# Kernel optimization log

Measured on AMD Instinct MI355X. Metric: run time of the kernel, lower is better.

## Reference

```python
import jax, jax.numpy as jnp
import numpy as np

H = 512

def _lstm_cell(x, h, c, Wih, Whh, bih, bhh):
    # PyTorch LSTMCell: gates ordered i, f, g, o
    g = x @ Wih.T + bih + h @ Whh.T + bhh
    i, f, gg, o = jnp.split(g, 4, axis=-1)
    i = jax.nn.sigmoid(i)
    f = jax.nn.sigmoid(f)
    gg = jnp.tanh(gg)
    o = jax.nn.sigmoid(o)
    c_new = f * c + i * gg
    h_new = o * jnp.tanh(c_new)
    return h_new, c_new


def setup_inputs() -> dict:
    key = jax.random.key(0)
    ks = jax.random.split(key, 12)
    B, T = 16, 6574
    s1 = 1.0 / np.sqrt(H)
    u = lambda k, shape: jax.random.uniform(k, shape, jnp.float32, -s1, s1)
    return {
        "input": jax.random.normal(ks[0], (B, T, 2), jnp.float32),
        "W_ih1": u(ks[1], (4 * H, 2)),
        "W_hh1": u(ks[2], (4 * H, H)),
        "b_ih1": u(ks[3], (4 * H,)),
        "b_hh1": u(ks[4], (4 * H,)),
        "W_ih2": u(ks[5], (4 * H, H)),
        "W_hh2": u(ks[6], (4 * H, H)),
        "b_ih2": u(ks[7], (4 * H,)),
        "b_hh2": u(ks[8], (4 * H,)),
        "W_out": u(ks[9], (1, H)),
        "b_out": u(ks[10], (1,)),
    }


def reference(input, W_ih1, W_hh1, b_ih1, b_hh1, W_ih2, W_hh2, b_ih2, b_hh2, W_out, b_out):
    B = input.shape[0]
    h1 = jnp.zeros((B, H), input.dtype)
    c1 = jnp.zeros((B, H), input.dtype)
    h2 = jnp.zeros((B, H), input.dtype)
    c2 = jnp.zeros((B, H), input.dtype)

    def step(carry, x_t):
        h1, c1, h2, c2 = carry
        h1, c1 = _lstm_cell(x_t, h1, c1, W_ih1, W_hh1, b_ih1, b_hh1)
        h2, c2 = _lstm_cell(h1, h2, c2, W_ih2, W_hh2, b_ih2, b_hh2)
        out_t = h2 @ W_out.T + b_out  # [B, 1]
        return (h1, c1, h2, c2), out_t

    xs = jnp.swapaxes(input, 0, 1)  # [T, B, 2]
    _, outs = jax.lax.scan(step, (h1, c1, h2, c2), xs)
    return jnp.swapaxes(outs, 0, 1)  # [B, T, 1]
```

## Files before the change

kernel.cpp:

```cpp
#include <hip/hip_runtime.h>
#include <math.h>

#define NWG  256
#define NTHR 256
#define AGT __HIP_MEMORY_SCOPE_AGENT

#define O_W2  0
#define O_W1  16384
#define O_U   24576
#define O_WX  33280
#define O_B1  33312
#define O_B2  33328
#define O_WO  33344
#define O_XS  33348
#define O_G1  33364
#define O_G2  33492
#define O_C1  33620
#define O_C2  33652
#define LDS_FLOATS 33684

union U64F2 { unsigned long long u; float f[2]; };

__global__ void ws_init_kernel(unsigned* flags, float* h1g, float* h2g,
                               float* out, const float* bout, int n_out) {
    int i = blockIdx.x * blockDim.x + threadIdx.x;
    int n = gridDim.x * blockDim.x;
    float bo = bout[0];
    for (int j = i; j < NWG; j += n) flags[j] = 0u;
    for (int j = i; j < 16384; j += n) { h1g[j] = 0.0f; h2g[j] = 0.0f; }
    for (int j = i; j < n_out; j += n) out[j] = bo;
}

__device__ __forceinline__ float sigm(float x) { return 1.0f / (1.0f + __expf(-x)); }
__device__ __forceinline__ float tanh_fast(float x) { return 2.0f / (1.0f + __expf(-2.0f * x)) - 1.0f; }

__device__ __forceinline__ void gbar(unsigned* flags, int wg, int tid, unsigned ph) {
    __syncthreads();
    asm volatile("s_waitcnt vmcnt(0)" ::: "memory");
    const int half = wg & 1;
    if (tid == 0)
        __hip_atomic_store(&flags[(half << 7) + (wg >> 1)], ph, __ATOMIC_RELAXED, AGT);
    if (tid < 32) {
        const unsigned long long* f64 = (const unsigned long long*)flags + (half << 6);
        bool done;
        do {
            unsigned long long v0 = __hip_atomic_load(&f64[2 * tid],     __ATOMIC_RELAXED, AGT);
            unsigned long long v1 = __hip_atomic_load(&f64[2 * tid + 1], __ATOMIC_RELAXED, AGT);
            done = ((unsigned)v0 >= ph) && ((unsigned)(v0 >> 32) >= ph) &&
                   ((unsigned)v1 >= ph) && ((unsigned)(v1 >> 32) >= ph);
            if (!__all(done)) __builtin_amdgcn_s_sleep(1);
        } while (!__all(done));
    }
    __syncthreads();
}

__global__ __launch_bounds__(NTHR, 1) void lstm_kernel(
    const float* __restrict__ xin,  const float* __restrict__ Wih1,
    const float* __restrict__ Whh1, const float* __restrict__ bih1,
    const float* __restrict__ bhh1, const float* __restrict__ Wih2,
    const float* __restrict__ Whh2, const float* __restrict__ bih2,
    const float* __restrict__ bhh2, const float* __restrict__ Wout,
    const float* __restrict__ bout, float* __restrict__ out,
    unsigned* __restrict__ flags, float* __restrict__ h1g,
    float* __restrict__ h2g, float* __restrict__ outred, int T)
{
    __shared__ float lds[LDS_FLOATS];
    const int tid = threadIdx.x;
    const int wg  = blockIdx.x;
    const int bh  = wg & 1;
    const int jg  = wg >> 1;
    const int j0  = jg * 4;
    const int bd  = bh * 8 + (jg & 7);
    const int jh  = jg >> 3;

    for (int idx = tid; idx < 2048; idx += NTHR) {
        int r = idx >> 7, c4 = idx & 127;
        int grow = (r >> 2) * 512 + j0 + (r & 3);
        *(float4*)&lds[O_W1 + r * 512 + c4 * 4] = *(const float4*)&Whh1[grow * 512 + c4 * 4];
    }
    for (int idx = tid; idx < 4096; idx += NTHR) {
        int r = idx >> 8, c4 = idx & 255;
        int grow = (r >> 2) * 512 + j0 + (r & 3);
        int k = c4 * 4;
        const float* src = (k < 512) ? &Wih2[grow * 512 + k] : &Whh2[grow * 512 + (k - 512)];
        *(float4*)&lds[O_W2 + r * 1024 + k] = *(const float4*)src;
    }
    if (tid < 32) {
        int r = tid >> 1, grow = (r >> 2) * 512 + j0 + (r & 3);
        lds[O_WX + tid] = Wih1[grow * 2 + (tid & 1)];
    }
    if (tid < 16) {
        int grow = (tid >> 2) * 512 + j0 + (tid & 3);
        lds[O_B1 + tid] = bih1[grow] + bhh1[grow];
        lds[O_B2 + tid] = bih2[grow] + bhh2[grow];
    }
    if (tid < 4) lds[O_WO + tid] = Wout[j0 + tid];
    if (tid < 32) { lds[O_C1 + tid] = 0.0f; lds[O_C2 + tid] = 0.0f; }
    __syncthreads();

    const int wv = tid >> 6;
    const int ks = tid & 63;
    unsigned ph = 0;

    float xreg = 0.0f;
    if (tid < 16 && T > 0) {
        int b = tid >> 1, cm = tid & 1;
        xreg = xin[((bh * 8 + b) * (long)T + 0) * 2 + cm];
    }

    for (int s = 0; s <= T; ++s) {
        const int p = s & 1, pq = p ^ 1;

        if (s >= 2 && tid == 0) {
            const unsigned long long* row64 =
                (const unsigned long long*)(outred + pq * 2048 + bd * 128 + jh * 8);
            U64F2 v0; v0.u = __hip_atomic_load(&row64[0], __ATOMIC_RELAXED, AGT);
            U64F2 v1; v1.u = __hip_atomic_load(&row64[1], __ATOMIC_RELAXED, AGT);
            U64F2 v2; v2.u = __hip_atomic_load(&row64[2], __ATOMIC_RELAXED, AGT);
            U64F2 v3; v3.u = __hip_atomic_load(&row64[3], __ATOMIC_RELAXED, AGT);
            float sum = (v0.f[0] + v0.f[1]) + (v1.f[0] + v1.f[1])
                      + (v2.f[0] + v2.f[1]) + (v3.f[0] + v3.f[1]);
            atomicAdd(&out[bd * T + (s - 2)], sum);
        }

        if (tid < 16) {
            if (s < T) lds[O_XS + tid] = xreg;
            if (s + 1 < T) {
                int b = tid >> 1, cm = tid & 1;
                xreg = xin[((bh * 8 + b) * (long)T + (s + 1)) * 2 + cm];
            }
        }

        {
            const float* srcb = (tid < 128)
                ? (h1g + pq * 8192 + (bh * 8) * 512 + tid * 4)
                : (h2g + pq * 8192 + (bh * 8) * 512 + (tid - 128) * 4);
            float4 r0, r1, r2, r3, r4, r5, r6, r7;
            asm volatile(
                "global_load_dwordx4 %0, %8, off sc0 sc1\n\t"
                "global_load_dwordx4 %1, %9, off sc0 sc1\n\t"
                "global_load_dwordx4 %2, %10, off sc0 sc1\n\t"
                "global_load_dwordx4 %3, %11, off sc0 sc1\n\t"
                "global_load_dwordx4 %4, %12, off sc0 sc1\n\t"
                "global_load_dwordx4 %5, %13, off sc0 sc1\n\t"
                "global_load_dwordx4 %6, %14, off sc0 sc1\n\t"
                "global_load_dwordx4 %7, %15, off sc0 sc1\n\t"
                "s_waitcnt vmcnt(0)"
                : "=&v"(r0), "=&v"(r1), "=&v"(r2), "=&v"(r3),
                  "=&v"(r4), "=&v"(r5), "=&v"(r6), "=&v"(r7)
                : "v"(srcb),        "v"(srcb + 512),  "v"(srcb + 1024), "v"(srcb + 1536),
                  "v"(srcb + 2048), "v"(srcb + 2560), "v"(srcb + 3072), "v"(srcb + 3584)
                : "memory");
            const int d = tid * 4;
            *(float4*)&lds[O_U + 0 * 1024 + d] = r0;
            *(float4*)&lds[O_U + 1 * 1024 + d] = r1;
            *(float4*)&lds[O_U + 2 * 1024 + d] = r2;
            *(float4*)&lds[O_U + 3 * 1024 + d] = r3;
            *(float4*)&lds[O_U + 4 * 1024 + d] = r4;
            *(float4*)&lds[O_U + 5 * 1024 + d] = r5;
            *(float4*)&lds[O_U + 6 * 1024 + d] = r6;
            *(float4*)&lds[O_U + 7 * 1024 + d] = r7;
        }
        __syncthreads();

        float a1[4][8], a2[4][8];
        #pragma unroll
        for (int r = 0; r < 4; ++r)
            #pragma unroll
            for (int b = 0; b < 8; ++b) { a1[r][b] = 0.0f; a2[r][b] = 0.0f; }
        {
            const float* W2b = &lds[O_W2 + wv * 4096];
            const float* W1b = &lds[O_W1 + wv * 2048];
            #pragma unroll
            for (int c = 0; c < 4; ++c) {
                const int k = ks * 4 + c * 256;
                float4 u0 = *(const float4*)&W2b[k];
                float4 u1 = *(const float4*)&W2b[1024 + k];
                float4 u2 = *(const float4*)&W2b[2048 + k];
                float4 u3 = *(const float4*)&W2b[3072 + k];
                float4 w0, w1, w2, w3;
                if (c < 2) {
                    w0 = *(const float4*)&W1b[k];
                    w1 = *(const float4*)&W1b[512 + k];
                    w2 = *(const float4*)&W1b[1024 + k];
                    w3 = *(const float4*)&W1b[1536 + k];
                }
                #pragma unroll
                for (int b = 0; b < 8; ++b) {
                    float4 h = *(const float4*)&lds[O_U + b * 1024 + k];
                    a2[0][b] = fmaf(u0.x,h.x,fmaf(u0.y,h.y,fmaf(u0.z,h.z,fmaf(u0.w,h.w,a2[0][b]))));
                    a2[1][b] = fmaf(u1.x,h.x,fmaf(u1.y,h.y,fmaf(u1.z,h.z,fmaf(u1.w,h.w,a2[1][b]))));
                    a2[2][b] = fmaf(u2.x,h.x,fmaf(u2.y,h.y,fmaf(u2.z,h.z,fmaf(u2.w,h.w,a2[2][b]))));
                    a2[3][b] = fmaf(u3.x,h.x,fmaf(u3.y,h.y,fmaf(u3.z,h.z,fmaf(u3.w,h.w,a2[3][b]))));
                    if (c < 2) {
                        a1[0][b] = fmaf(w0.x,h.x,fmaf(w0.y,h.y,fmaf(w0.z,h.z,fmaf(w0.w,h.w,a1[0][b]))));
                        a1[1][b] = fmaf(w1.x,h.x,fmaf(w1.y,h.y,fmaf(w1.z,h.z,fmaf(w1.w,h.w,a1[1][b]))));
                        a1[2][b] = fmaf(w2.x,h.x,fmaf(w2.y,h.y,fmaf(w2.z,h.z,fmaf(w2.w,h.w,a1[2][b]))));
                        a1[3][b] = fmaf(w3.x,h.x,fmaf(w3.y,h.y,fmaf(w3.z,h.z,fmaf(w3.w,h.w,a1[3][b]))));
                    }
                }
            }
        }
        __syncthreads();

        #pragma unroll
        for (int r = 0; r < 4; ++r)
            #pragma unroll
            for (int b = 0; b < 8; ++b)
                lds[O_U + ((wv * 4 + r) * 8 + b) * 68 + ks] = a1[r][b];
        __syncthreads();
        {
            int o = tid >> 1, hf = tid & 1;
            const float* rr = &lds[O_U + o * 68 + hf * 32];
            float sum = 0.0f;
            #pragma unroll
            for (int c = 0; c < 8; ++c) { float4 v = *(const float4*)&rr[c * 4]; sum += v.x + v.y + v.z + v.w; }
            sum += __shfl_xor(sum, 1);
            if (hf == 0) {
                int r = o >> 3, b = o & 7;
                float g = sum + lds[O_B1 + r]
                        + lds[O_WX + r * 2]     * lds[O_XS + b * 2]
                        + lds[O_WX + r * 2 + 1] * lds[O_XS + b * 2 + 1];
                lds[O_G1 + o] = (wv == 2) ? tanh_fast(g) : sigm(g);
            }
        }
        __syncthreads();

        if (tid < 32 && s < T) {
            int jj = tid >> 3, b = tid & 7;
            float gi = lds[O_G1 + (0 * 4 + jj) * 8 + b];
            float gf = lds[O_G1 + (1 * 4 + jj) * 8 + b];
            float gg = lds[O_G1 + (2 * 4 + jj) * 8 + b];
            float go = lds[O_G1 + (3 * 4 + jj) * 8 + b];
            float c  = gf * lds[O_C1 + tid] + gi * gg;
            lds[O_C1 + tid] = c;
            __hip_atomic_store(&h1g[p * 8192 + (bh * 8 + b) * 512 + j0 + jj],
                               go * tanh_fast(c), __ATOMIC_RELAXED, AGT);
        }

        #pragma unroll
        for (int r = 0; r < 4; ++r)
            #pragma unroll
            for (int b = 0; b < 8; ++b)
                lds[O_U + ((wv * 4 + r) * 8 + b) * 68 + ks] = a2[r][b];
        __syncthreads();
        {
            int o = tid >> 1, hf = tid & 1;
            const float* rr = &lds[O_U + o * 68 + hf * 32];
            float sum = 0.0f;
            #pragma unroll
            for (int c = 0; c < 8; ++c) { float4 v = *(const float4*)&rr[c * 4]; sum += v.x + v.y + v.z + v.w; }
            sum += __shfl_xor(sum, 1);
            if (hf == 0) {
                float g = sum + lds[O_B2 + (o >> 3)];
                lds[O_G2 + o] = (wv == 2) ? tanh_fast(g) : sigm(g);
            }
        }
        __syncthreads();

        if (tid >= 32 && tid < 64 && s >= 1) {
            int t2 = tid - 32, jj = t2 >> 3, b = t2 & 7;
            float gi = lds[O_G2 + (0 * 4 + jj) * 8 + b];
            float gf = lds[O_G2 + (1 * 4 + jj) * 8 + b];
            float gg = lds[O_G2 + (2 * 4 + jj) * 8 + b];
            float go = lds[O_G2 + (3 * 4 + jj) * 8 + b];
            float c  = gf * lds[O_C2 + t2] + gi * gg;
            lds[O_C2 + t2] = c;
            float h = go * tanh_fast(c);
            __hip_atomic_store(&h2g[p * 8192 + (bh * 8 + b) * 512 + j0 + jj],
                               h, __ATOMIC_RELAXED, AGT);
            float hn = lds[O_WO + jj] * h;
            hn += __shfl_xor(hn, 8);
            hn += __shfl_xor(hn, 16);
            if (jj == 0)
                __hip_atomic_store(&outred[p * 2048 + (bh * 8 + b) * 128 + jg],
                                   hn, __ATOMIC_RELAXED, AGT);
        }

        gbar(flags, wg, tid, ++ph);
    }

    if (tid == 0) {
        const unsigned long long* row64 =
            (const unsigned long long*)(outred + (T & 1) * 2048 + bd * 128 + jh * 8);
        U64F2 v0; v0.u = __hip_atomic_load(&row64[0], __ATOMIC_RELAXED, AGT);
        U64F2 v1; v1.u = __hip_atomic_load(&row64[1], __ATOMIC_RELAXED, AGT);
        U64F2 v2; v2.u = __hip_atomic_load(&row64[2], __ATOMIC_RELAXED, AGT);
        U64F2 v3; v3.u = __hip_atomic_load(&row64[3], __ATOMIC_RELAXED, AGT);
        float sum = (v0.f[0] + v0.f[1]) + (v1.f[0] + v1.f[1])
                  + (v2.f[0] + v2.f[1]) + (v3.f[0] + v3.f[1]);
        atomicAdd(&out[bd * T + (T - 1)], sum);
    }
}

extern "C" void kernel_launch(void* const* d_in, const int* in_sizes, int n_in,
                              void* d_out, int out_size, void* d_ws, size_t ws_size,
                              hipStream_t stream) {
    const float* xin  = (const float*)d_in[0];
    const float* Wih1 = (const float*)d_in[1];
    const float* Whh1 = (const float*)d_in[2];
    const float* bih1 = (const float*)d_in[3];
    const float* bhh1 = (const float*)d_in[4];
    const float* Wih2 = (const float*)d_in[5];
    const float* Whh2 = (const float*)d_in[6];
    const float* bih2 = (const float*)d_in[7];
    const float* bhh2 = (const float*)d_in[8];
    const float* Wout = (const float*)d_in[9];
    const float* bout = (const float*)d_in[10];
    float* outp = (float*)d_out;
    int T = in_sizes[0] / 32;

    unsigned* flags = (unsigned*)d_ws;
    float* h1g    = (float*)d_ws + 4096;
    float* h2g    = h1g + 16384;
    float* outredp= h2g + 16384;

    hipLaunchKernelGGL(ws_init_kernel, dim3(64), dim3(256), 0, stream,
                       flags, h1g, h2g, outp, bout, out_size);

    hipLaunchKernelGGL(lstm_kernel, dim3(NWG), dim3(NTHR), 0, stream,
                       xin, Wih1, Whh1, bih1, bhh1, Wih2, Whh2, bih2, bhh2,
                       Wout, bout, outp, flags, h1g, h2g, outredp, T);
}
```

Baseline: 53.99 ms.

## Prefetch next-step h1 into LDS via early per-layer flag before global barrier

```diff
diff --git a/kernel.cpp b/kernel.cpp
--- a/kernel.cpp
+++ b/kernel.cpp
@@ -26,7 +26,7 @@
     int i = blockIdx.x * blockDim.x + threadIdx.x;
     int n = gridDim.x * blockDim.x;
     float bo = bout[0];
-    for (int j = i; j < NWG; j += n) flags[j] = 0u;
+    for (int j = i; j < 512; j += n) flags[j] = 0u;
     for (int j = i; j < 16384; j += n) { h1g[j] = 0.0f; h2g[j] = 0.0f; }
     for (int j = i; j < n_out; j += n) out[j] = bo;
 }
@@ -53,6 +53,24 @@
     }
     __syncthreads();
 }
+
+#define STAGE8(srcb, r0,r1,r2,r3,r4,r5,r6,r7)                            \
+    asm volatile(                                                         \
+        "global_load_dwordx4 %0, %8, off sc0 sc1\n\t"                     \
+        "global_load_dwordx4 %1, %9, off sc0 sc1\n\t"                     \
+        "global_load_dwordx4 %2, %10, off sc0 sc1\n\t"                    \
+        "global_load_dwordx4 %3, %11, off sc0 sc1\n\t"                    \
+        "global_load_dwordx4 %4, %12, off sc0 sc1\n\t"                    \
+        "global_load_dwordx4 %5, %13, off sc0 sc1\n\t"                    \
+        "global_load_dwordx4 %6, %14, off sc0 sc1\n\t"                    \
+        "global_load_dwordx4 %7, %15, off sc0 sc1\n\t"                    \
+        "s_waitcnt vmcnt(0)"                                              \
+        : "=&v"(r0), "=&v"(r1), "=&v"(r2), "=&v"(r3),                     \
+          "=&v"(r4), "=&v"(r5), "=&v"(r6), "=&v"(r7)                      \
+        : "v"(srcb),        "v"(srcb + 512),  "v"(srcb + 1024),           \
+          "v"(srcb + 1536), "v"(srcb + 2048), "v"(srcb + 2560),           \
+          "v"(srcb + 3072), "v"(srcb + 3584)                              \
+        : "memory")
 
 __global__ __launch_bounds__(NTHR, 1) void lstm_kernel(
     const float* __restrict__ xin,  const float* __restrict__ Wih1,
@@ -72,6 +90,7 @@
     const int j0  = jg * 4;
     const int bd  = bh * 8 + (jg & 7);
     const int jh  = jg >> 3;
+    unsigned* flagsA = flags + 256;
 
     for (int idx = tid; idx < 2048; idx += NTHR) {
         int r = idx >> 7, c4 = idx & 127;
@@ -96,6 +115,21 @@
     }
     if (tid < 4) lds[O_WO + tid] = Wout[j0 + tid];
     if (tid < 32) { lds[O_C1 + tid] = 0.0f; lds[O_C2 + tid] = 0.0f; }
+
+    if (tid >= 128) {
+        const float* srcb = h1g + 1 * 8192 + (bh * 8) * 512 + (tid - 128) * 4;
+        float4 r0, r1, r2, r3, r4, r5, r6, r7;
+        STAGE8(srcb, r0, r1, r2, r3, r4, r5, r6, r7);
+        const int d = (tid - 128) * 4;
+        *(float4*)&lds[O_U + 0 * 1024 + d] = r0;
+        *(float4*)&lds[O_U + 1 * 1024 + d] = r1;
+        *(float4*)&lds[O_U + 2 * 1024 + d] = r2;
+        *(float4*)&lds[O_U + 3 * 1024 + d] = r3;
+        *(float4*)&lds[O_U + 4 * 1024 + d] = r4;
+        *(float4*)&lds[O_U + 5 * 1024 + d] = r5;
+        *(float4*)&lds[O_U + 6 * 1024 + d] = r6;
+        *(float4*)&lds[O_U + 7 * 1024 + d] = r7;
+    }
     __syncthreads();
 
     const int wv = tid >> 6;
@@ -131,27 +165,11 @@
             }
         }
 
-        {
-            const float* srcb = (tid < 128)
-                ? (h1g + pq * 8192 + (bh * 8) * 512 + tid * 4)
-                : (h2g + pq * 8192 + (bh * 8) * 512 + (tid - 128) * 4);
+        if (tid < 128) {
+            const float* srcb = h2g + pq * 8192 + (bh * 8) * 512 + tid * 4;
             float4 r0, r1, r2, r3, r4, r5, r6, r7;
-            asm volatile(
-                "global_load_dwordx4 %0, %8, off sc0 sc1\n\t"
-                "global_load_dwordx4 %1, %9, off sc0 sc1\n\t"
-                "global_load_dwordx4 %2, %10, off sc0 sc1\n\t"
-                "global_load_dwordx4 %3, %11, off sc0 sc1\n\t"
-                "global_load_dwordx4 %4, %12, off sc0 sc1\n\t"
-                "global_load_dwordx4 %5, %13, off sc0 sc1\n\t"
-                "global_load_dwordx4 %6, %14, off sc0 sc1\n\t"
-                "global_load_dwordx4 %7, %15, off sc0 sc1\n\t"
-                "s_waitcnt vmcnt(0)"
-                : "=&v"(r0), "=&v"(r1), "=&v"(r2), "=&v"(r3),
-                  "=&v"(r4), "=&v"(r5), "=&v"(r6), "=&v"(r7)
-                : "v"(srcb),        "v"(srcb + 512),  "v"(srcb + 1024), "v"(srcb + 1536),
-                  "v"(srcb + 2048), "v"(srcb + 2560), "v"(srcb + 3072), "v"(srcb + 3584)
-                : "memory");
-            const int d = tid * 4;
+            STAGE8(srcb, r0, r1, r2, r3, r4, r5, r6, r7);
+            const int d = 512 + tid * 4;
             *(float4*)&lds[O_U + 0 * 1024 + d] = r0;
             *(float4*)&lds[O_U + 1 * 1024 + d] = r1;
             *(float4*)&lds[O_U + 2 * 1024 + d] = r2;
@@ -243,6 +261,13 @@
             #pragma unroll
             for (int b = 0; b < 8; ++b)
                 lds[O_U + ((wv * 4 + r) * 8 + b) * 68 + ks] = a2[r][b];
+
+        if (tid < 64 && s < T) {
+            asm volatile("s_waitcnt vmcnt(0)" ::: "memory");
+            if (tid == 0)
+                __hip_atomic_store(&flagsA[((wg & 1) << 7) + (wg >> 1)],
+                                   (unsigned)(s + 1), __ATOMIC_RELAXED, AGT);
+        }
         __syncthreads();
         {
             int o = tid >> 1, hf = tid & 1;
@@ -277,6 +302,31 @@
                                    hn, __ATOMIC_RELAXED, AGT);
         }
 
+        if (tid >= 128 && s < T) {
+            const unsigned long long* fA64 =
+                (const unsigned long long*)flagsA + ((wg & 1) << 6);
+            const unsigned tgt = (unsigned)(s + 1);
+            int l = tid & 63;
+            bool ok;
+            do {
+                unsigned long long v = __hip_atomic_load(&fA64[l], __ATOMIC_RELAXED, AGT);
+                ok = ((unsigned)v >= tgt) && ((unsigned)(v >> 32) >= tgt);
+                if (!__all(ok)) __builtin_amdgcn_s_sleep(1);
+            } while (!__all(ok));
+            const float* srcb = h1g + p * 8192 + (bh * 8) * 512 + (tid - 128) * 4;
+            float4 r0, r1, r2, r3, r4, r5, r6, r7;
+            STAGE8(srcb, r0, r1, r2, r3, r4, r5, r6, r7);
+            const int d = (tid - 128) * 4;
+            *(float4*)&lds[O_U + 0 * 1024 + d] = r0;
+            *(float4*)&lds[O_U + 1 * 1024 + d] = r1;
+            *(float4*)&lds[O_U + 2 * 1024 + d] = r2;
+            *(float4*)&lds[O_U + 3 * 1024 + d] = r3;
+            *(float4*)&lds[O_U + 4 * 1024 + d] = r4;
+            *(float4*)&lds[O_U + 5 * 1024 + d] = r5;
+            *(float4*)&lds[O_U + 6 * 1024 + d] = r6;
+            *(float4*)&lds[O_U + 7 * 1024 + d] = r7;
+        }
+
         gbar(flags, wg, tid, ++ph);
     }
 
```

Result: no change. 53.54 ms, median of 2 (-0.8%).
